# Performance work log

Measured on AMD Instinct MI355X. Metric: run time of the kernel, lower is better.

The kernel has to match this reference:

```python
import jax, jax.numpy as jnp
import numpy as np

N_NODES = 50000
N_EDGES = 800000
N_GRAPHS = 512
F_IN = 128
D = 256
EPS = 1e-5
NEG_SLOPE = 0.01  # torch LeakyReLU default


def leaky_relu(x):
    return jnp.where(x >= 0, x, NEG_SLOPE * x)


def egnn_conv(x, edge_index, edge_attr, lin2_w, lin2_b, lin_w, lin_b, n_nodes):
    # message: LeakyReLU(lin(x_j + lin2(edge_attr))), aggregate: add at target i
    src, dst = edge_index[0], edge_index[1]
    ea = edge_attr @ lin2_w.T + lin2_b          # [E, in]
    msg = (x[src] + ea) @ lin_w.T + lin_b        # [E, out]
    msg = leaky_relu(msg)
    return jax.ops.segment_sum(msg, dst, num_segments=n_nodes)


def batch_norm(x, w, b):
    # training-mode BatchNorm1d: biased batch statistics over node axis
    mean = jnp.mean(x, axis=0)
    var = jnp.mean(jnp.square(x - mean), axis=0)
    return (x - mean) * jax.lax.rsqrt(var + EPS) * w + b


def setup_inputs() -> dict:
    key = jax.random.key(0)
    ks = jax.random.split(key, 8)
    inp = {
        "node_ids": jax.random.randint(ks[0], (N_NODES,), 0, 51),
        "edge_index": jax.random.randint(ks[1], (2, N_EDGES), 0, N_NODES),
        "edge_attr": jax.random.normal(ks[2], (N_EDGES, 4), dtype=jnp.float32),
        "batch": jnp.sort(jax.random.randint(ks[3], (N_NODES,), 0, N_GRAPHS)),
        "emb_table": jax.random.normal(ks[4], (51, F_IN), dtype=jnp.float32) * 0.1,
        "c1_lin2_w": jax.random.normal(ks[5], (F_IN, 4), dtype=jnp.float32) * 0.1,
        "c1_lin2_b": jnp.zeros((F_IN,), jnp.float32),
        "c1_lin_w": jax.random.normal(ks[6], (D, F_IN), dtype=jnp.float32) * (1.0 / np.sqrt(F_IN)),
        "c1_lin_b": jnp.zeros((D,), jnp.float32),
        "bn1_w": jnp.ones((D,), jnp.float32),
        "bn1_b": jnp.zeros((D,), jnp.float32),
        "c2_lin2_w": jax.random.normal(jax.random.fold_in(key, 10), (D, 4), dtype=jnp.float32) * 0.1,
        "c2_lin2_b": jnp.zeros((D,), jnp.float32),
        "c2_lin_w": jax.random.normal(ks[7], (D, D), dtype=jnp.float32) * (1.0 / np.sqrt(D)),
        "c2_lin_b": jnp.zeros((D,), jnp.float32),
        "bn2_w": jnp.ones((D,), jnp.float32),
        "bn2_b": jnp.zeros((D,), jnp.float32),
        "gate_w": jax.random.normal(jax.random.fold_in(key, 11), (1, D), dtype=jnp.float32) * 0.1,
        "gate_b": jnp.zeros((1,), jnp.float32),
    }
    return inp


def reference(node_ids, edge_index, edge_attr, batch, emb_table,
              c1_lin2_w, c1_lin2_b, c1_lin_w, c1_lin_b, bn1_w, bn1_b,
              c2_lin2_w, c2_lin2_b, c2_lin_w, c2_lin_b, bn2_w, bn2_b,
              gate_w, gate_b):
    x = emb_table[node_ids]                                   # [N, F_IN]
    x = egnn_conv(x, edge_index, edge_attr, c1_lin2_w, c1_lin2_b,
                  c1_lin_w, c1_lin_b, N_NODES)                # [N, D]
    x = leaky_relu(batch_norm(x, bn1_w, bn1_b))
    x2 = egnn_conv(x, edge_index, edge_attr, c2_lin2_w, c2_lin2_b,
                   c2_lin_w, c2_lin_b, N_NODES)               # [N, D]
    x2 = leaky_relu(batch_norm(x2, bn2_w, bn2_b))
    # AttentionalAggregation: softmax of gate over each graph segment
    gate = x2 @ gate_w.T + gate_b                             # [N, 1]
    gmax = jax.ops.segment_max(gate, batch, num_segments=N_GRAPHS)
    e = jnp.exp(gate - gmax[batch])                           # [N, 1]
    denom = jax.ops.segment_sum(e, batch, num_segments=N_GRAPHS)
    alpha = e / denom[batch]
    out = jax.ops.segment_sum(alpha * x2, batch, num_segments=N_GRAPHS)
    return out                                                # [G, D]
```

## Files before the change

### kernel.cpp

```cpp
#include <hip/hip_runtime.h>
#include <hip/hip_bf16.h>

#define NN 50000
#define NE 800000
#define NG 512

typedef __bf16 bf16_t;
typedef __bf16 bf16x8 __attribute__((ext_vector_type(8)));
typedef __bf16 bf16x4 __attribute__((ext_vector_type(4)));
typedef float f32x4 __attribute__((ext_vector_type(4)));
typedef float f32x2 __attribute__((ext_vector_type(2)));

__device__ __forceinline__ float lrelu(float v) { return v >= 0.f ? v : 0.01f * v; }

__device__ __forceinline__ f32x2 unpk2(unsigned w) {
    union { unsigned u; float f; } lo, hi;
    lo.u = w << 16;
    hi.u = w & 0xffff0000u;
    f32x2 r; r[0] = lo.f; r[1] = hi.f; return r;
}

__device__ __forceinline__ int vzero() {
    int vz;
    asm("v_mov_b32 %0, 0" : "=v"(vz));
    return vz;
}

__global__ void gme_setup(const float* __restrict__ emb,
                          const float* __restrict__ c1lw, const float* __restrict__ c1l2w,
                          const float* __restrict__ c1l2b, const float* __restrict__ c1lb,
                          const float* __restrict__ c2lw, const float* __restrict__ c2l2w,
                          const float* __restrict__ c2l2b, const float* __restrict__ c2lb,
                          bf16_t* __restrict__ TYB, float* __restrict__ WC1,
                          float* __restrict__ WC2, float* __restrict__ CB2,
                          bf16_t* __restrict__ W2B) {
    int b = blockIdx.x, t = threadIdx.x;
    if (b < 51) {
        const float4* er = (const float4*)(emb + b * 128);
        const float4* zb = (const float4*)c1l2b;
        const float4* wr = (const float4*)(c1lw + t * 128);
        float s = 0.f;
        for (int k = 0; k < 32; ++k) {
            float4 e = er[k], z = zb[k], w = wr[k];
            s += (e.x + z.x) * w.x + (e.y + z.y) * w.y + (e.z + z.z) * w.z + (e.w + z.w) * w.w;
        }
        TYB[b * 256 + t] = (bf16_t)(s + c1lb[t]);
    } else if (b == 51) {
        const float4* wr = (const float4*)(c1lw + t * 128);
        const float4* cw = (const float4*)c1l2w;
        float4 a = make_float4(0.f, 0.f, 0.f, 0.f);
        for (int k = 0; k < 32; ++k) {
            float4 w = wr[k];
            float4 c0 = cw[k * 4 + 0], c1 = cw[k * 4 + 1], c2 = cw[k * 4 + 2], c3 = cw[k * 4 + 3];
            a.x += w.x * c0.x + w.y * c1.x + w.z * c2.x + w.w * c3.x;
            a.y += w.x * c0.y + w.y * c1.y + w.z * c2.y + w.w * c3.y;
            a.z += w.x * c0.z + w.y * c1.z + w.z * c2.z + w.w * c3.z;
            a.w += w.x * c0.w + w.y * c1.w + w.z * c2.w + w.w * c3.w;
        }
        ((float4*)WC1)[t] = a;
    } else if (b == 52) {
        const float4* wr = (const float4*)(c2lw + t * 256);
        const float4* cw = (const float4*)c2l2w;
        const float4* zb = (const float4*)c2l2b;
        float4 a = make_float4(0.f, 0.f, 0.f, 0.f);
        float ab = 0.f;
        for (int k = 0; k < 64; ++k) {
            float4 w = wr[k];
            float4 c0 = cw[k * 4 + 0], c1 = cw[k * 4 + 1], c2 = cw[k * 4 + 2], c3 = cw[k * 4 + 3];
            float4 z = zb[k];
            a.x += w.x * c0.x + w.y * c1.x + w.z * c2.x + w.w * c3.x;
            a.y += w.x * c0.y + w.y * c1.y + w.z * c2.y + w.w * c3.y;
            a.z += w.x * c0.z + w.y * c1.z + w.z * c2.z + w.w * c3.z;
            a.w += w.x * c0.w + w.y * c1.w + w.z * c2.w + w.w * c3.w;
            ab += w.x * z.x + w.y * z.y + w.z * z.z + w.w * z.w;
        }
        ((float4*)WC2)[t] = a;
        CB2[t] = ab + c2lb[t];
    } else {
        int i0 = (b - 53) * 1024;
        for (int r = 0; r < 4; ++r) {
            int i = i0 + r * 256 + t;
            W2B[i] = (bf16_t)c2lw[i];
        }
    }
}

__global__ void gme_count(const int* __restrict__ ei, int* __restrict__ cnt) {
    int e = blockIdx.x * 256 + threadIdx.x;
    if (e >= NE) return;
    atomicAdd(&cnt[ei[NE + e]], 1);
}

__global__ void gme_scan1(const int* __restrict__ CNT, int* __restrict__ LP,
                          int* __restrict__ BS) {
    __shared__ int lds[256];
    int b = blockIdx.x, t = threadIdx.x;
    int i = b * 196 + t;
    int v = (t < 196 && i < NN) ? CNT[i] : 0;
    lds[t] = v;
    __syncthreads();
    for (int off = 1; off < 256; off <<= 1) {
        int u = (t >= off) ? lds[t - off] : 0;
        __syncthreads();
        lds[t] += u;
        __syncthreads();
    }
    if (t < 196 && i < NN) LP[i] = lds[t] - v;
    if (t == 255) BS[b] = lds[255];
}

__global__ void gme_scan2(const int* __restrict__ BS, int* __restrict__ BX,
                          int* __restrict__ RS) {
    __shared__ int lds[256];
    int t = threadIdx.x;
    int v = BS[t];
    lds[t] = v;
    __syncthreads();
    for (int off = 1; off < 256; off <<= 1) {
        int u = (t >= off) ? lds[t - off] : 0;
        __syncthreads();
        lds[t] += u;
        __syncthreads();
    }
    BX[t] = lds[t] - v;
    if (t == 255) RS[NN] = lds[255];
}

__global__ void gme_scan3(const int* __restrict__ LP, const int* __restrict__ BX,
                          int* __restrict__ RS, int* __restrict__ CUR) {
    int b = blockIdx.x, t = threadIdx.x;
    if (t >= 196) return;
    int i = b * 196 + t;
    if (i >= NN) return;
    int v = BX[b] + LP[i];
    RS[i] = v;
    CUR[i] = v;
}

__global__ void gme_scatter(const int* __restrict__ ei,
                            const float4* __restrict__ eattr,
                            const int* __restrict__ node_ids,
                            int* __restrict__ CUR, uint4* __restrict__ SE) {
    int e = blockIdx.x * 256 + threadIdx.x;
    if (e >= NE) return;
    int s = ei[e];
    int d = ei[NE + e];
    int nid = node_ids[s];
    float4 at = eattr[e];
    union { bf16_t h[2]; unsigned u; } p01, p23;
    p01.h[0] = (bf16_t)at.x; p01.h[1] = (bf16_t)at.y;
    p23.h[0] = (bf16_t)at.z; p23.h[1] = (bf16_t)at.w;
    int pos = atomicAdd(&CUR[d], 1);
    SE[pos] = make_uint4((unsigned)(s | (nid << 16)), p01.u, p23.u, 0u);
}

__global__ __launch_bounds__(256) void gme_conv0(
        const int* __restrict__ RS, const uint4* __restrict__ SE,
        const bf16_t* __restrict__ TYB, const float* __restrict__ Wc,
        float* __restrict__ agg) {
    __shared__ __align__(16) uint2 sTY[51 * 64];
    {
        const uint4* s4 = (const uint4*)TYB;
        uint4* d4 = (uint4*)sTY;
        for (int i = threadIdx.x; i < 51 * 32; i += 256) d4[i] = s4[i];
    }
    __syncthreads();
    int lane = threadIdx.x & 63;
    int vz = vzero();
    const float4* wc4 = (const float4*)Wc;
    int c4 = lane * 4;
    float4 w0 = wc4[c4 + 0], w1 = wc4[c4 + 1], w2 = wc4[c4 + 2], w3 = wc4[c4 + 3];
    f32x2 wA0 = {w0.x, w1.x}, wB0 = {w0.y, w1.y}, wC0 = {w0.z, w1.z}, wD0 = {w0.w, w1.w};
    f32x2 wA1 = {w2.x, w3.x}, wB1 = {w2.y, w3.y}, wC1 = {w2.z, w3.z}, wD1 = {w2.w, w3.w};
    const f32x2 zero = {0.f, 0.f};
    const uint2* lrow = sTY + lane;
    int base = blockIdx.x * 16 + (threadIdx.x >> 6) * 4;
#pragma unroll 1
    for (int k = 0; k < 4; ++k) {
        int node = __builtin_amdgcn_readfirstlane(base + k);
        int rs = RS[node], re = RS[node + 1];
        f32x2 accP0 = zero, accP1 = zero, accA0 = zero, accA1 = zero;
        auto accum = [&](uint4 se, uint2 r) {
            f32x2 y0 = unpk2(r.x), y1 = unpk2(r.y);
            f32x2 axy = unpk2(se.y), azw = unpk2(se.z);
            f32x2 ax = {axy[0], axy[0]}, ay = {axy[1], axy[1]};
            f32x2 az = {azw[0], azw[0]}, aw = {azw[1], azw[1]};
            f32x2 m0 = __builtin_elementwise_fma(ax, wA0, y0);
            f32x2 m1 = __builtin_elementwise_fma(ax, wA1, y1);
            m0 = __builtin_elementwise_fma(ay, wB0, m0);
            m1 = __builtin_elementwise_fma(ay, wB1, m1);
            m0 = __builtin_elementwise_fma(az, wC0, m0);
            m1 = __builtin_elementwise_fma(az, wC1, m1);
            m0 = __builtin_elementwise_fma(aw, wD0, m0);
            m1 = __builtin_elementwise_fma(aw, wD1, m1);
            accA0 += m0; accA1 += m1;
            accP0 += __builtin_elementwise_max(m0, zero);
            accP1 += __builtin_elementwise_max(m1, zero);
        };
        int j = rs;
        for (; j + 8 <= re; j += 8) {
            uint4 se[8]; uint2 r[8];
#pragma unroll
            for (int u = 0; u < 8; ++u) se[u] = SE[j + u + vz];
#pragma unroll
            for (int u = 0; u < 8; ++u) r[u] = lrow[(se[u].x >> 16) << 6];
#pragma unroll
            for (int u = 0; u < 8; ++u) accum(se[u], r[u]);
        }
        if (j + 4 <= re) {
            uint4 se[4]; uint2 r[4];
#pragma unroll
            for (int u = 0; u < 4; ++u) se[u] = SE[j + u + vz];
#pragma unroll
            for (int u = 0; u < 4; ++u) r[u] = lrow[(se[u].x >> 16) << 6];
#pragma unroll
            for (int u = 0; u < 4; ++u) accum(se[u], r[u]);
            j += 4;
        }
        for (; j < re; ++j) {
            uint4 se = SE[j + vz];
            accum(se, lrow[(se.x >> 16) << 6]);
        }
        const f32x2 c99 = {0.99f, 0.99f}, c01 = {0.01f, 0.01f};
        f32x2 o0 = __builtin_elementwise_fma(accP0, c99, accA0 * c01);
        f32x2 o1 = __builtin_elementwise_fma(accP1, c99, accA1 * c01);
        *((float4*)(agg + node * 256) + lane) = make_float4(o0[0], o0[1], o1[0], o1[1]);
    }
}

__global__ __launch_bounds__(256, 4) void gme_conv1(
        const int* __restrict__ RS, const uint4* __restrict__ SE,
        const bf16_t* __restrict__ QB, const float* __restrict__ Wc,
        float* __restrict__ agg) {
    int lane = threadIdx.x & 63;
    int node = __builtin_amdgcn_readfirstlane(blockIdx.x * 4 + (threadIdx.x >> 6));
    if (node >= NN) return;
    const float4* wc4 = (const float4*)Wc;
    int c4 = lane * 4;
    float4 w0 = wc4[c4 + 0], w1 = wc4[c4 + 1], w2 = wc4[c4 + 2], w3 = wc4[c4 + 3];
    f32x2 wA0 = {w0.x, w1.x}, wB0 = {w0.y, w1.y}, wC0 = {w0.z, w1.z}, wD0 = {w0.w, w1.w};
    f32x2 wA1 = {w2.x, w3.x}, wB1 = {w2.y, w3.y}, wC1 = {w2.z, w3.z}, wD1 = {w2.w, w3.w};
    const f32x2 zero = {0.f, 0.f};
    f32x2 accP0 = zero, accP1 = zero, accA0 = zero, accA1 = zero;
    int rs = RS[node], re = RS[node + 1];
    const char* yb = (const char*)QB;
    unsigned loff = (unsigned)(lane << 3);
    auto rowld = [&](unsigned row) -> uint2 {
        return *(const uint2*)(yb + (row << 9) + loff);
    };
    auto accum = [&](uint4 se, uint2 r) {
        f32x2 y0 = unpk2(r.x), y1 = unpk2(r.y);
        f32x2 axy = unpk2(se.y), azw = unpk2(se.z);
        f32x2 ax = {axy[0], axy[0]}, ay = {axy[1], axy[1]};
        f32x2 az = {azw[0], azw[0]}, aw = {azw[1], azw[1]};
        f32x2 m0 = __builtin_elementwise_fma(ax, wA0, y0);
        f32x2 m1 = __builtin_elementwise_fma(ax, wA1, y1);
        m0 = __builtin_elementwise_fma(ay, wB0, m0);
        m1 = __builtin_elementwise_fma(ay, wB1, m1);
        m0 = __builtin_elementwise_fma(az, wC0, m0);
        m1 = __builtin_elementwise_fma(az, wC1, m1);
        m0 = __builtin_elementwise_fma(aw, wD0, m0);
        m1 = __builtin_elementwise_fma(aw, wD1, m1);
        accA0 += m0; accA1 += m1;
        accP0 += __builtin_elementwise_max(m0, zero);
        accP1 += __builtin_elementwise_max(m1, zero);
    };
    int j = rs;
    for (; j + 12 <= re; j += 12) {
        uint4 se[12]; uint2 r[12];
#pragma unroll
        for (int u = 0; u < 12; ++u) se[u] = SE[j + u];
#pragma unroll
        for (int u = 0; u < 12; ++u) r[u] = rowld(se[u].x & 0xffffu);
#pragma unroll
        for (int u = 0; u < 12; ++u) accum(se[u], r[u]);
    }
    if (j + 8 <= re) {
        uint4 se[8]; uint2 r[8];
#pragma unroll
        for (int u = 0; u < 8; ++u) se[u] = SE[j + u];
#pragma unroll
        for (int u = 0; u < 8; ++u) r[u] = rowld(se[u].x & 0xffffu);
#pragma unroll
        for (int u = 0; u < 8; ++u) accum(se[u], r[u]);
        j += 8;
    }
    if (j + 4 <= re) {
        uint4 se[4]; uint2 r[4];
#pragma unroll
        for (int u = 0; u < 4; ++u) se[u] = SE[j + u];
#pragma unroll
        for (int u = 0; u < 4; ++u) r[u] = rowld(se[u].x & 0xffffu);
#pragma unroll
        for (int u = 0; u < 4; ++u) accum(se[u], r[u]);
        j += 4;
    }
    for (; j < re; ++j) {
        uint4 se = SE[j];
        accum(se, rowld(se.x & 0xffffu));
    }
    const f32x2 c99 = {0.99f, 0.99f}, c01 = {0.01f, 0.01f};
    f32x2 o0 = __builtin_elementwise_fma(accP0, c99, accA0 * c01);
    f32x2 o1 = __builtin_elementwise_fma(accP1, c99, accA1 * c01);
    *((float4*)(agg + node * 256) + lane) = make_float4(o0[0], o0[1], o1[0], o1[1]);
}

__global__ __launch_bounds__(256) void gme_bns1(const float* __restrict__ P,
                                                float* __restrict__ PART) {
    __shared__ float ls[4][256], lq[4][256];
    int lane = threadIdx.x & 63;
    int w = threadIdx.x >> 6;
    int b = blockIdx.x;
    int r0 = b * 98;
    int r1 = r0 + 98; if (r1 > NN) r1 = NN;
    float4 s = make_float4(0, 0, 0, 0), q = make_float4(0, 0, 0, 0);
    for (int n = r0 + w; n < r1; n += 4) {
        float4 v = ((const float4*)P)[n * 64 + lane];
        s.x += v.x; s.y += v.y; s.z += v.z; s.w += v.w;
        q.x += v.x * v.x; q.y += v.y * v.y; q.z += v.z * v.z; q.w += v.w * v.w;
    }
    int c = lane * 4;
    ls[w][c] = s.x; ls[w][c + 1] = s.y; ls[w][c + 2] = s.z; ls[w][c + 3] = s.w;
    lq[w][c] = q.x; lq[w][c + 1] = q.y; lq[w][c + 2] = q.z; lq[w][c + 3] = q.w;
    __syncthreads();
    if (w == 0) {
#pragma unroll
        for (int k = 0; k < 4; ++k) {
            int cc = c + k;
            PART[b * 512 + cc] = ls[0][cc] + ls[1][cc] + ls[2][cc] + ls[3][cc];
            PART[b * 512 + 256 + cc] = lq[0][cc] + lq[1][cc] + lq[2][cc] + lq[3][cc];
        }
    }
}

__global__ __launch_bounds__(512) void gme_bns2(const float* __restrict__ PART,
                                                float* __restrict__ ST) {
    int t = threadIdx.x;
    int b = blockIdx.x;
    float acc = 0.f;
#pragma unroll
    for (int r = 0; r < 32; ++r) acc += PART[(b * 32 + r) * 512 + t];
    atomicAdd(&ST[t], acc);
}

__global__ __launch_bounds__(256) void gme_gemm(const float* __restrict__ P,
                                                const float* __restrict__ ST,
                                                const float* __restrict__ bw,
                                                const float* __restrict__ bb,
                                                const bf16_t* __restrict__ W2B,
                                                const float* __restrict__ CB2,
                                                bf16_t* __restrict__ QB) {
    __shared__ float s_sc[256], s_sh[256];
    __shared__ __align__(16) uint4 sB[8192];
    {
        int c = threadIdx.x;
        float mean = ST[c] * (1.f / NN);
        float var = ST[256 + c] * (1.f / NN) - mean * mean;
        float sc = bw[c] * rsqrtf(var + 1e-5f);
        s_sc[c] = sc;
        s_sh[c] = bb[c] - mean * sc;
        const uint4* w4 = (const uint4*)W2B;
#pragma unroll
        for (int it = 0; it < 32; ++it) {
            int i = it * 256 + c;
            int row = i >> 5, slot = i & 31;
            sB[(row << 5) | (slot ^ (row & 7))] = w4[i];
        }
    }
    __syncthreads();
    int lane = threadIdx.x & 63;
    int wave = blockIdx.x * 4 + (threadIdx.x >> 6);
    if (wave >= NN / 16) return;
    int m0 = wave * 16;
    int r = lane & 15, q = lane >> 4;
    int rx = r & 7;
    const float* arow = P + (m0 + r) * 256 + q * 8;
    bf16x8 a[8];
#pragma unroll
    for (int kt = 0; kt < 8; ++kt) {
        int k0 = kt * 32 + q * 8;
        float4 u0 = *(const float4*)(arow + kt * 32);
        float4 u1 = *(const float4*)(arow + kt * 32 + 4);
        bf16x8 f;
        f[0] = (bf16_t)lrelu(fmaf(u0.x, s_sc[k0 + 0], s_sh[k0 + 0]));
        f[1] = (bf16_t)lrelu(fmaf(u0.y, s_sc[k0 + 1], s_sh[k0 + 1]));
        f[2] = (bf16_t)lrelu(fmaf(u0.z, s_sc[k0 + 2], s_sh[k0 + 2]));
        f[3] = (bf16_t)lrelu(fmaf(u0.w, s_sc[k0 + 3], s_sh[k0 + 3]));
        f[4] = (bf16_t)lrelu(fmaf(u1.x, s_sc[k0 + 4], s_sh[k0 + 4]));
        f[5] = (bf16_t)lrelu(fmaf(u1.y, s_sc[k0 + 5], s_sh[k0 + 5]));
        f[6] = (bf16_t)lrelu(fmaf(u1.z, s_sc[k0 + 6], s_sh[k0 + 6]));
        f[7] = (bf16_t)lrelu(fmaf(u1.w, s_sc[k0 + 7], s_sh[k0 + 7]));
        a[kt] = f;
    }
#pragma unroll 1
    for (int g = 0; g < 2; ++g) {
        f32x4 acc[8];
#pragma unroll
        for (int n8 = 0; n8 < 8; ++n8) acc[n8] = (f32x4){0.f, 0.f, 0.f, 0.f};
#pragma unroll
        for (int kt = 0; kt < 8; ++kt) {
            int slot = (kt * 4 + q) ^ rx;
            bf16x8 bf[8];
#pragma unroll
            for (int n8 = 0; n8 < 8; ++n8) {
                int row = g * 128 + n8 * 16 + r;
                bf[n8] = *(const bf16x8*)&sB[(row << 5) | slot];
            }
#pragma unroll
            for (int n8 = 0; n8 < 8; ++n8) {
                acc[n8] = __builtin_amdgcn_mfma_f32_16x16x32_bf16(bf[n8], a[kt], acc[n8], 0, 0, 0);
            }
        }
#pragma unroll
        for (int n8 = 0; n8 < 8; ++n8) {
            int nt = g * 8 + n8;
            float4 cbv = ((const float4*)CB2)[nt * 4 + q];
            bf16x4 o;
            o[0] = (bf16_t)(acc[n8][0] + cbv.x);
            o[1] = (bf16_t)(acc[n8][1] + cbv.y);
            o[2] = (bf16_t)(acc[n8][2] + cbv.z);
            o[3] = (bf16_t)(acc[n8][3] + cbv.w);
            *(bf16x4*)(QB + (m0 + r) * 256 + nt * 16 + q * 4) = o;
        }
    }
}

__global__ void gme_gstart(const int* __restrict__ batch, int* __restrict__ GS) {
    int n = blockIdx.x * 256 + threadIdx.x;
    if (n >= NN) return;
    int b = batch[n];
    if (n == 0) {
        for (int g = 0; g <= b; ++g) GS[g] = 0;
    } else {
        int a = batch[n - 1];
        for (int g = a + 1; g <= b; ++g) GS[g] = n;
    }
    if (n == NN - 1) {
        for (int g = b + 1; g <= NG; ++g) GS[g] = NN;
    }
}

__global__ __launch_bounds__(256) void gme_attn(const int* __restrict__ GS,
                                                const float* __restrict__ P,
                                                const float* __restrict__ ST,
                                                const float* __restrict__ bw,
                                                const float* __restrict__ bb,
                                                const float* __restrict__ gw,
                                                const float* __restrict__ gb,
                                                float* __restrict__ out) {
    __shared__ float gl[1024];
    __shared__ float rr[8];
    int g = blockIdx.x, t = threadIdx.x;
    int lo = GS[g], hi = GS[g + 1];
    if (lo >= hi) { out[g * 256 + t] = 0.f; return; }
    int lane = t & 63, w = t >> 6;
    {
        float4 s4 = ((const float4*)ST)[lane];
        float4 q4 = ((const float4*)(ST + 256))[lane];
        float4 w4 = ((const float4*)bw)[lane];
        float4 b4 = ((const float4*)bb)[lane];
        float4 g4 = ((const float4*)gw)[lane];
        float m0 = s4.x * (1.f / NN), m1 = s4.y * (1.f / NN);
        float m2 = s4.z * (1.f / NN), m3 = s4.w * (1.f / NN);
        float sc0 = w4.x * rsqrtf(q4.x * (1.f / NN) - m0 * m0 + 1e-5f);
        float sc1 = w4.y * rsqrtf(q4.y * (1.f / NN) - m1 * m1 + 1e-5f);
        float sc2 = w4.z * rsqrtf(q4.z * (1.f / NN) - m2 * m2 + 1e-5f);
        float sc3 = w4.w * rsqrtf(q4.w * (1.f / NN) - m3 * m3 + 1e-5f);
        float sh0 = b4.x - m0 * sc0, sh1 = b4.y - m1 * sc1;
        float sh2 = b4.z - m2 * sc2, sh3 = b4.w - m3 * sc3;
        float gb0 = gb[0];
        for (int n = lo + w; n < hi; n += 4) {
            float4 p = *(const float4*)(P + n * 256 + lane * 4);
            float d = lrelu(fmaf(p.x, sc0, sh0)) * g4.x
                    + lrelu(fmaf(p.y, sc1, sh1)) * g4.y
                    + lrelu(fmaf(p.z, sc2, sh2)) * g4.z
                    + lrelu(fmaf(p.w, sc3, sh3)) * g4.w;
#pragma unroll
            for (int off = 32; off > 0; off >>= 1) d += __shfl_xor(d, off, 64);
            if (lane == 0) gl[n - lo] = d + gb0;
        }
    }
    __syncthreads();
    int cnt = hi - lo;
    float lm = -3.0e38f;
    for (int i = t; i < cnt; i += 256) lm = fmaxf(lm, gl[i]);
#pragma unroll
    for (int off = 32; off > 0; off >>= 1) lm = fmaxf(lm, __shfl_xor(lm, off, 64));
    if (lane == 0) rr[w] = lm;
    __syncthreads();
    float mx = fmaxf(fmaxf(rr[0], rr[1]), fmaxf(rr[2], rr[3]));
    float ls = 0.f;
    for (int i = t; i < cnt; i += 256) { float e = expf(gl[i] - mx); gl[i] = e; ls += e; }
#pragma unroll
    for (int off = 32; off > 0; off >>= 1) ls += __shfl_xor(ls, off, 64);
    if (lane == 0) rr[4 + w] = ls;
    __syncthreads();
    float sinv = 1.f / (rr[4] + rr[5] + rr[6] + rr[7]);
    float mean = ST[t] * (1.f / NN);
    float var = ST[256 + t] * (1.f / NN) - mean * mean;
    float sc = bw[t] * rsqrtf(var + 1e-5f);
    float sh = bb[t] - mean * sc;
    float a0 = 0.f, a1 = 0.f, a2 = 0.f, a3 = 0.f;
    int n = lo;
    for (; n + 4 <= hi; n += 4) {
        float p0 = P[n * 256 + t], p1 = P[(n + 1) * 256 + t];
        float p2 = P[(n + 2) * 256 + t], p3 = P[(n + 3) * 256 + t];
        a0 = fmaf(gl[n - lo + 0], lrelu(fmaf(p0, sc, sh)), a0);
        a1 = fmaf(gl[n - lo + 1], lrelu(fmaf(p1, sc, sh)), a1);
        a2 = fmaf(gl[n - lo + 2], lrelu(fmaf(p2, sc, sh)), a2);
        a3 = fmaf(gl[n - lo + 3], lrelu(fmaf(p3, sc, sh)), a3);
    }
    for (; n < hi; ++n) a0 = fmaf(gl[n - lo], lrelu(fmaf(P[n * 256 + t], sc, sh)), a0);
    out[g * 256 + t] = (a0 + a1 + a2 + a3) * sinv;
}

extern "C" void kernel_launch(void* const* d_in, const int* in_sizes, int n_in,
                              void* d_out, int out_size, void* d_ws, size_t ws_size,
                              hipStream_t stream) {
    const int* node_ids = (const int*)d_in[0];
    const int* edge_index = (const int*)d_in[1];
    const float4* edge_attr = (const float4*)d_in[2];
    const int* batch = (const int*)d_in[3];
    const float* emb = (const float*)d_in[4];
    const float* c1l2w = (const float*)d_in[5];
    const float* c1l2b = (const float*)d_in[6];
    const float* c1lw = (const float*)d_in[7];
    const float* c1lb = (const float*)d_in[8];
    const float* bn1w = (const float*)d_in[9];
    const float* bn1b = (const float*)d_in[10];
    const float* c2l2w = (const float*)d_in[11];
    const float* c2l2b = (const float*)d_in[12];
    const float* c2lw = (const float*)d_in[13];
    const float* c2lb = (const float*)d_in[14];
    const float* bn2w = (const float*)d_in[15];
    const float* bn2b = (const float*)d_in[16];
    const float* gate_w = (const float*)d_in[17];
    const float* gate_b = (const float*)d_in[18];

    char* ws = (char*)d_ws;
    size_t oP = 0;
    size_t oQB = oP + 51200000;
    size_t oSE = oQB + 25600000;
    size_t oRS = oSE + 12800000;
    size_t oCNT = oRS + 200064;
    size_t oCUR = oCNT + 200000;
    size_t oLP = oCUR + 200000;
    size_t oBS = oLP + 200000;
    size_t oBX = oBS + 1024;
    size_t oTY = oBX + 1024;
    size_t oWC1 = oTY + 52224;
    size_t oWC2 = oWC1 + 4096;
    size_t oCB2 = oWC2 + 4096;
    size_t oW2B = oCB2 + 1024;
    size_t oST = oW2B + 131072;
    size_t oGS = oST + 4096;
    size_t oPART = oGS + 2064;

    float* P = (float*)(ws + oP);
    bf16_t* QB = (bf16_t*)(ws + oQB);
    uint4* SE = (uint4*)(ws + oSE);
    int* RS = (int*)(ws + oRS);
    int* CNT = (int*)(ws + oCNT);
    int* CUR = (int*)(ws + oCUR);
    int* LP = (int*)(ws + oLP);
    int* BS = (int*)(ws + oBS);
    int* BX = (int*)(ws + oBX);
    bf16_t* TYB = (bf16_t*)(ws + oTY);
    float* WC1 = (float*)(ws + oWC1);
    float* WC2 = (float*)(ws + oWC2);
    float* CB2 = (float*)(ws + oCB2);
    bf16_t* W2B = (bf16_t*)(ws + oW2B);
    float* ST1 = (float*)(ws + oST);
    float* ST2 = ST1 + 512;
    int* GS = (int*)(ws + oGS);
    float* PART = (float*)(ws + oPART);

    hipMemsetAsync(CNT, 0, NN * sizeof(int), stream);
    hipMemsetAsync(ST1, 0, 4096, stream);

    gme_setup<<<117, 256, 0, stream>>>(emb, c1lw, c1l2w, c1l2b, c1lb,
                                       c2lw, c2l2w, c2l2b, c2lb,
                                       TYB, WC1, WC2, CB2, W2B);
    gme_count<<<NE / 256, 256, 0, stream>>>(edge_index, CNT);
    gme_scan1<<<256, 256, 0, stream>>>(CNT, LP, BS);
    gme_scan2<<<1, 256, 0, stream>>>(BS, BX, RS);
    gme_scan3<<<256, 256, 0, stream>>>(LP, BX, RS, CUR);
    gme_scatter<<<NE / 256, 256, 0, stream>>>(edge_index, edge_attr, node_ids,
                                              CUR, SE);
    gme_gstart<<<(NN + 255) / 256, 256, 0, stream>>>(batch, GS);
    gme_conv0<<<NN / 16, 256, 0, stream>>>(RS, SE, TYB, WC1, P);
    gme_bns1<<<512, 256, 0, stream>>>(P, PART);
    gme_bns2<<<16, 512, 0, stream>>>(PART, ST1);
    gme_gemm<<<(NN / 16 + 3) / 4, 256, 0, stream>>>(P, ST1, bn1w, bn1b, W2B, CB2, QB);
    gme_conv1<<<NN / 4, 256, 0, stream>>>(RS, SE, QB, WC2, P);
    gme_bns1<<<512, 256, 0, stream>>>(P, PART);
    gme_bns2<<<16, 512, 0, stream>>>(PART, ST2);
    gme_attn<<<NG, 256, 0, stream>>>(GS, P, ST2, bn2w, bn2b, gate_w, gate_b,
                                     (float*)d_out);
}
```

Before: 405.0 us.

## Fuse BatchNorm statistics into conv kernels and fold small setup kernels together

Each conv kernel now computes per-column sum and sum-of-squares in LDS and atomically adds them into 256 partial rows. A small reduction kernel (gme_bred) replaces the two-pass bns1/bns2 statistics kernels, so P no longer has to be re-read from memory for statistics. The CNT memset moves into extra blocks of gme_setup and the graph-start computation moves into gme_scan3, removing launches. In exchange there are float atomics, which make the reduction order nondeterministic, plus an extra LDS reduction with a barrier in each conv block.

```diff
diff --git a/kernel.cpp b/kernel.cpp
--- a/kernel.cpp
+++ b/kernel.cpp
@@ -33,7 +33,7 @@
                           const float* __restrict__ c2l2b, const float* __restrict__ c2lb,
                           bf16_t* __restrict__ TYB, float* __restrict__ WC1,
                           float* __restrict__ WC2, float* __restrict__ CB2,
-                          bf16_t* __restrict__ W2B) {
+                          bf16_t* __restrict__ W2B, int* __restrict__ CNT) {
     int b = blockIdx.x, t = threadIdx.x;
     if (b < 51) {
         const float4* er = (const float4*)(emb + b * 128);
@@ -76,12 +76,15 @@
         }
         ((float4*)WC2)[t] = a;
         CB2[t] = ab + c2lb[t];
-    } else {
+    } else if (b < 117) {
         int i0 = (b - 53) * 1024;
         for (int r = 0; r < 4; ++r) {
             int i = i0 + r * 256 + t;
             W2B[i] = (bf16_t)c2lw[i];
         }
+    } else {
+        int i = (b - 117) * 256 + t;
+        if (i < NN) CNT[i] = 0;
     }
 }
 
@@ -127,7 +130,8 @@
 }
 
 __global__ void gme_scan3(const int* __restrict__ LP, const int* __restrict__ BX,
-                          int* __restrict__ RS, int* __restrict__ CUR) {
+                          int* __restrict__ RS, int* __restrict__ CUR,
+                          const int* __restrict__ batch, int* __restrict__ GS) {
     int b = blockIdx.x, t = threadIdx.x;
     if (t >= 196) return;
     int i = b * 196 + t;
@@ -135,6 +139,16 @@
     int v = BX[b] + LP[i];
     RS[i] = v;
     CUR[i] = v;
+    int bb = batch[i];
+    if (i == 0) {
+        for (int g = 0; g <= bb; ++g) GS[g] = 0;
+    } else {
+        int a = batch[i - 1];
+        for (int g = a + 1; g <= bb; ++g) GS[g] = i;
+    }
+    if (i == NN - 1) {
+        for (int g = bb + 1; g <= NG; ++g) GS[g] = NN;
+    }
 }
 
 __global__ void gme_scatter(const int* __restrict__ ei,
@@ -157,7 +171,7 @@
 __global__ __launch_bounds__(256) void gme_conv0(
         const int* __restrict__ RS, const uint4* __restrict__ SE,
         const bf16_t* __restrict__ TYB, const float* __restrict__ Wc,
-        float* __restrict__ agg) {
+        float* __restrict__ agg, float* __restrict__ PARTS) {
     __shared__ __align__(16) uint2 sTY[51 * 64];
     {
         const uint4* s4 = (const uint4*)TYB;
@@ -166,6 +180,7 @@
     }
     __syncthreads();
     int lane = threadIdx.x & 63;
+    int w = threadIdx.x >> 6;
     int vz = vzero();
     const float4* wc4 = (const float4*)Wc;
     int c4 = lane * 4;
@@ -174,7 +189,8 @@
     f32x2 wA1 = {w2.x, w3.x}, wB1 = {w2.y, w3.y}, wC1 = {w2.z, w3.z}, wD1 = {w2.w, w3.w};
     const f32x2 zero = {0.f, 0.f};
     const uint2* lrow = sTY + lane;
-    int base = blockIdx.x * 16 + (threadIdx.x >> 6) * 4;
+    int base = blockIdx.x * 16 + w * 4;
+    f32x2 ssum0 = zero, ssum1 = zero, qsum0 = zero, qsum1 = zero;
 #pragma unroll 1
     for (int k = 0; k < 4; ++k) {
         int node = __builtin_amdgcn_readfirstlane(base + k);
@@ -225,16 +241,32 @@
         f32x2 o0 = __builtin_elementwise_fma(accP0, c99, accA0 * c01);
         f32x2 o1 = __builtin_elementwise_fma(accP1, c99, accA1 * c01);
         *((float4*)(agg + node * 256) + lane) = make_float4(o0[0], o0[1], o1[0], o1[1]);
-    }
+        ssum0 += o0; ssum1 += o1;
+        qsum0 += o0 * o0; qsum1 += o1 * o1;
+    }
+    __syncthreads();
+    float* red = (float*)sTY;
+    red[w * 512 + c4 + 0] = ssum0[0]; red[w * 512 + c4 + 1] = ssum0[1];
+    red[w * 512 + c4 + 2] = ssum1[0]; red[w * 512 + c4 + 3] = ssum1[1];
+    red[w * 512 + 256 + c4 + 0] = qsum0[0]; red[w * 512 + 256 + c4 + 1] = qsum0[1];
+    red[w * 512 + 256 + c4 + 2] = qsum1[0]; red[w * 512 + 256 + c4 + 3] = qsum1[1];
+    __syncthreads();
+    int cc = threadIdx.x;
+    float s = red[cc] + red[512 + cc] + red[1024 + cc] + red[1536 + cc];
+    float q = red[256 + cc] + red[768 + cc] + red[1280 + cc] + red[1792 + cc];
+    int prow = (blockIdx.x & 255) * 512;
+    atomicAdd(&PARTS[prow + cc], s);
+    atomicAdd(&PARTS[prow + 256 + cc], q);
 }
 
 __global__ __launch_bounds__(256, 4) void gme_conv1(
         const int* __restrict__ RS, const uint4* __restrict__ SE,
         const bf16_t* __restrict__ QB, const float* __restrict__ Wc,
-        float* __restrict__ agg) {
+        float* __restrict__ agg, float* __restrict__ PARTS) {
+    __shared__ float red[2048];
     int lane = threadIdx.x & 63;
-    int node = __builtin_amdgcn_readfirstlane(blockIdx.x * 4 + (threadIdx.x >> 6));
-    if (node >= NN) return;
+    int w = threadIdx.x >> 6;
+    int node = __builtin_amdgcn_readfirstlane(blockIdx.x * 4 + w);
     const float4* wc4 = (const float4*)Wc;
     int c4 = lane * 4;
     float4 w0 = wc4[c4 + 0], w1 = wc4[c4 + 1], w2 = wc4[c4 + 2], w3 = wc4[c4 + 3];
@@ -303,44 +335,33 @@
     f32x2 o0 = __builtin_elementwise_fma(accP0, c99, accA0 * c01);
     f32x2 o1 = __builtin_elementwise_fma(accP1, c99, accA1 * c01);
     *((float4*)(agg + node * 256) + lane) = make_float4(o0[0], o0[1], o1[0], o1[1]);
-}
-
-__global__ __launch_bounds__(256) void gme_bns1(const float* __restrict__ P,
-                                                float* __restrict__ PART) {
-    __shared__ float ls[4][256], lq[4][256];
-    int lane = threadIdx.x & 63;
-    int w = threadIdx.x >> 6;
-    int b = blockIdx.x;
-    int r0 = b * 98;
-    int r1 = r0 + 98; if (r1 > NN) r1 = NN;
-    float4 s = make_float4(0, 0, 0, 0), q = make_float4(0, 0, 0, 0);
-    for (int n = r0 + w; n < r1; n += 4) {
-        float4 v = ((const float4*)P)[n * 64 + lane];
-        s.x += v.x; s.y += v.y; s.z += v.z; s.w += v.w;
-        q.x += v.x * v.x; q.y += v.y * v.y; q.z += v.z * v.z; q.w += v.w * v.w;
-    }
-    int c = lane * 4;
-    ls[w][c] = s.x; ls[w][c + 1] = s.y; ls[w][c + 2] = s.z; ls[w][c + 3] = s.w;
-    lq[w][c] = q.x; lq[w][c + 1] = q.y; lq[w][c + 2] = q.z; lq[w][c + 3] = q.w;
-    __syncthreads();
-    if (w == 0) {
-#pragma unroll
-        for (int k = 0; k < 4; ++k) {
-            int cc = c + k;
-            PART[b * 512 + cc] = ls[0][cc] + ls[1][cc] + ls[2][cc] + ls[3][cc];
-            PART[b * 512 + 256 + cc] = lq[0][cc] + lq[1][cc] + lq[2][cc] + lq[3][cc];
-        }
-    }
-}
-
-__global__ __launch_bounds__(512) void gme_bns2(const float* __restrict__ PART,
-                                                float* __restrict__ ST) {
+    red[w * 512 + c4 + 0] = o0[0]; red[w * 512 + c4 + 1] = o0[1];
+    red[w * 512 + c4 + 2] = o1[0]; red[w * 512 + c4 + 3] = o1[1];
+    red[w * 512 + 256 + c4 + 0] = o0[0] * o0[0];
+    red[w * 512 + 256 + c4 + 1] = o0[1] * o0[1];
+    red[w * 512 + 256 + c4 + 2] = o1[0] * o1[0];
+    red[w * 512 + 256 + c4 + 3] = o1[1] * o1[1];
+    __syncthreads();
+    int cc = threadIdx.x;
+    float s = red[cc] + red[512 + cc] + red[1024 + cc] + red[1536 + cc];
+    float q = red[256 + cc] + red[768 + cc] + red[1280 + cc] + red[1792 + cc];
+    int prow = (blockIdx.x & 255) * 512;
+    atomicAdd(&PARTS[prow + cc], s);
+    atomicAdd(&PARTS[prow + 256 + cc], q);
+}
+
+__global__ __launch_bounds__(512) void gme_bred(float* __restrict__ PARTS,
+                                                float* __restrict__ ST, int zero) {
     int t = threadIdx.x;
     int b = blockIdx.x;
     float acc = 0.f;
 #pragma unroll
-    for (int r = 0; r < 32; ++r) acc += PART[(b * 32 + r) * 512 + t];
+    for (int r = 0; r < 16; ++r) acc += PARTS[(b * 16 + r) * 512 + t];
     atomicAdd(&ST[t], acc);
+    if (zero) {
+#pragma unroll
+        for (int r = 0; r < 16; ++r) PARTS[(b * 16 + r) * 512 + t] = 0.f;
+    }
 }
 
 __global__ __launch_bounds__(256) void gme_gemm(const float* __restrict__ P,
@@ -422,21 +443,6 @@
             o[3] = (bf16_t)(acc[n8][3] + cbv.w);
             *(bf16x4*)(QB + (m0 + r) * 256 + nt * 16 + q * 4) = o;
         }
-    }
-}
-
-__global__ void gme_gstart(const int* __restrict__ batch, int* __restrict__ GS) {
-    int n = blockIdx.x * 256 + threadIdx.x;
-    if (n >= NN) return;
-    int b = batch[n];
-    if (n == 0) {
-        for (int g = 0; g <= b; ++g) GS[g] = 0;
-    } else {
-        int a = batch[n - 1];
-        for (int g = a + 1; g <= b; ++g) GS[g] = n;
-    }
-    if (n == NN - 1) {
-        for (int g = b + 1; g <= NG; ++g) GS[g] = NN;
     }
 }
 
@@ -553,8 +559,8 @@
     size_t oCB2 = oWC2 + 4096;
     size_t oW2B = oCB2 + 1024;
     size_t oST = oW2B + 131072;
-    size_t oGS = oST + 4096;
-    size_t oPART = oGS + 2064;
+    size_t oPARTS = oST + 4096;
+    size_t oGS = oPARTS + 524288;
 
     float* P = (float*)(ws + oP);
     bf16_t* QB = (bf16_t*)(ws + oQB);
@@ -572,29 +578,25 @@
     bf16_t* W2B = (bf16_t*)(ws + oW2B);
     float* ST1 = (float*)(ws + oST);
     float* ST2 = ST1 + 512;
+    float* PARTS = (float*)(ws + oPARTS);
     int* GS = (int*)(ws + oGS);
-    float* PART = (float*)(ws + oPART);
-
-    hipMemsetAsync(CNT, 0, NN * sizeof(int), stream);
-    hipMemsetAsync(ST1, 0, 4096, stream);
-
-    gme_setup<<<117, 256, 0, stream>>>(emb, c1lw, c1l2w, c1l2b, c1lb,
+
+    hipMemsetAsync(ST1, 0, 4096 + 524288, stream);
+
+    gme_setup<<<313, 256, 0, stream>>>(emb, c1lw, c1l2w, c1l2b, c1lb,
                                        c2lw, c2l2w, c2l2b, c2lb,
-                                       TYB, WC1, WC2, CB2, W2B);
+                                       TYB, WC1, WC2, CB2, W2B, CNT);
     gme_count<<<NE / 256, 256, 0, stream>>>(edge_index, CNT);
     gme_scan1<<<256, 256, 0, stream>>>(CNT, LP, BS);
     gme_scan2<<<1, 256, 0, stream>>>(BS, BX, RS);
-    gme_scan3<<<256, 256, 0, stream>>>(LP, BX, RS, CUR);
+    gme_scan3<<<256, 256, 0, stream>>>(LP, BX, RS, CUR, batch, GS);
     gme_scatter<<<NE / 256, 256, 0, stream>>>(edge_index, edge_attr, node_ids,
                                               CUR, SE);
-    gme_gstart<<<(NN + 255) / 256, 256, 0, stream>>>(batch, GS);
-    gme_conv0<<<NN / 16, 256, 0, stream>>>(RS, SE, TYB, WC1, P);
-    gme_bns1<<<512, 256, 0, stream>>>(P, PART);
-    gme_bns2<<<16, 512, 0, stream>>>(PART, ST1);
+    gme_conv0<<<NN / 16, 256, 0, stream>>>(RS, SE, TYB, WC1, P, PARTS);
+    gme_bred<<<16, 512, 0, stream>>>(PARTS, ST1, 1);
     gme_gemm<<<(NN / 16 + 3) / 4, 256, 0, stream>>>(P, ST1, bn1w, bn1b, W2B, CB2, QB);
-    gme_conv1<<<NN / 4, 256, 0, stream>>>(RS, SE, QB, WC2, P);
-    gme_bns1<<<512, 256, 0, stream>>>(P, PART);
-    gme_bns2<<<16, 512, 0, stream>>>(PART, ST2);
+    gme_conv1<<<NN / 4, 256, 0, stream>>>(RS, SE, QB, WC2, P, PARTS);
+    gme_bred<<<16, 512, 0, stream>>>(PARTS, ST2, 0);
     gme_attn<<<NG, 256, 0, stream>>>(GS, P, ST2, bn2w, bn2b, gate_w, gate_b,
                                      (float*)d_out);
 }
```

Measured after the change: 389.5 us. 3.8% less time.
